# Kernel optimization log

Hardware: AMD Instinct MI355X
Metric: run time of the kernel (lower is better)

Reference implementation:

```python
import jax, jax.numpy as jnp
import numpy as np

N_NODES = 50000
N_EDGES = 800000
IN_DIM = 128
HID_DIM = 64
OUT_DIM = 64
NUM_GRAPHS = 512


def setup_inputs() -> dict:
    key = jax.random.key(0)
    ks = jax.random.split(key, 8)
    x = jax.random.normal(ks[0], (N_NODES, IN_DIM), dtype=jnp.float32)
    edge_index = jax.random.randint(ks[1], (2, N_EDGES), 0, N_NODES, dtype=jnp.int64)
    batch = jnp.sort(jax.random.randint(ks[2], (N_NODES,), 0, NUM_GRAPHS, dtype=jnp.int64))
    s1 = 1.0 / np.sqrt(IN_DIM)
    s2 = 1.0 / np.sqrt(HID_DIM)
    W1 = jax.random.uniform(ks[3], (IN_DIM, HID_DIM), jnp.float32, -s1, s1)
    b1 = jax.random.uniform(ks[4], (HID_DIM,), jnp.float32, -s1, s1)
    W2 = jax.random.uniform(ks[5], (HID_DIM, OUT_DIM), jnp.float32, -s2, s2)
    b2 = jax.random.uniform(ks[6], (OUT_DIM,), jnp.float32, -s2, s2)
    return {"x": x, "edge_index": edge_index, "batch": batch,
            "W1": W1, "b1": b1, "W2": W2, "b2": b2}


def _gcn_layer(h, W, b, src, dst, norm, n_nodes):
    # linear transform first (keeps the per-edge gather at output width)
    h = h @ W + b                      # [N, d_out]
    msg = h[src] * norm[:, None]       # [E, d_out] gathered, normalized messages
    agg = jax.ops.segment_sum(msg, dst, num_segments=n_nodes)  # scatter-add
    return jax.nn.relu(agg)


def reference(x, edge_index, batch, W1, b1, W2, b2):
    src, dst = edge_index[0], edge_index[1]
    # symmetric degree normalization: deg^{-1/2}[src] * deg^{-1/2}[dst]
    deg = jax.ops.segment_sum(jnp.ones((src.shape[0],), x.dtype), dst,
                              num_segments=N_NODES)
    dinv = jax.lax.rsqrt(jnp.maximum(deg, 1.0))
    norm = dinv[src] * dinv[dst]       # [E]

    h = _gcn_layer(x, W1, b1, src, dst, norm, N_NODES)   # dropout = identity (eval)
    h = _gcn_layer(h, W2, b2, src, dst, norm, N_NODES)

    # scatter_mean pooling over batch indices
    sums = jax.ops.segment_sum(h, batch, num_segments=NUM_GRAPHS)
    cnts = jax.ops.segment_sum(jnp.ones((N_NODES,), h.dtype), batch,
                               num_segments=NUM_GRAPHS)
    return sums / jnp.maximum(cnts, 1.0)[:, None]        # [NUM_GRAPHS, OUT_DIM]
```

## Files before the change

kernel.cpp:

```cpp
#include <hip/hip_runtime.h>
#include <hip/hip_fp16.h>

#define N_NODES 50000
#define N_EDGES 800000
#define IN_DIM 128
#define HID_DIM 64
#define OUT_DIM 64
#define NUM_GRAPHS 512
#define CAP 64

typedef unsigned short u16;

__global__ __launch_bounds__(256) void gemm1_fill_kernel(
    const float* __restrict__ X, const float* __restrict__ W,
    const float* __restrict__ bias, __half* __restrict__ Yh, int n_nodes,
    const int* __restrict__ src, const int* __restrict__ dst,
    int* __restrict__ cursor, u16* __restrict__ ssorted, int n_edges) {
    __shared__ float xs[16][IN_DIM];
    const int tid = threadIdx.x;
    const int idx = blockIdx.x >> 1;

    if (blockIdx.x & 1) {
        int e = idx * 256 + tid;
        if (e < n_edges) {
            int d = dst[e];
            int pos = atomicAdd(&cursor[d], 1);
            if (pos < CAP)
                __builtin_nontemporal_store((u16)src[e],
                                            &ssorted[(size_t)d * CAP + pos]);
        }
        return;
    }

    const int base = idx * 16;
    const int nvec = 16 * IN_DIM / 4;
    const float4* X4 = reinterpret_cast<const float4*>(X + (size_t)base * IN_DIM);
    float4* xs4 = reinterpret_cast<float4*>(&xs[0][0]);
    for (int i = tid; i < nvec; i += 256) {
        int row = (i * 4) / IN_DIM;
        xs4[i] = (base + row < n_nodes) ? X4[i] : make_float4(0.f, 0.f, 0.f, 0.f);
    }
    __syncthreads();

    const int j = tid & 63;
    const int q = tid >> 6;
    float b = bias[j];
    float a0 = b, a1 = b, a2 = b, a3 = b;
#pragma unroll 4
    for (int k = 0; k < IN_DIM; ++k) {
        float w = W[k * 64 + j];
        a0 += w * xs[q * 4 + 0][k];
        a1 += w * xs[q * 4 + 1][k];
        a2 += w * xs[q * 4 + 2][k];
        a3 += w * xs[q * 4 + 3][k];
    }
    int n0 = base + q * 4;
    if (n0 + 0 < n_nodes) Yh[(size_t)(n0 + 0) * 64 + j] = __float2half(a0);
    if (n0 + 1 < n_nodes) Yh[(size_t)(n0 + 1) * 64 + j] = __float2half(a1);
    if (n0 + 2 < n_nodes) Yh[(size_t)(n0 + 2) * 64 + j] = __float2half(a2);
    if (n0 + 3 < n_nodes) Yh[(size_t)(n0 + 3) * 64 + j] = __float2half(a3);
}

__global__ __launch_bounds__(256) void scale_bounds_kernel(
    __half* __restrict__ H1h, const int* __restrict__ deg,
    float* __restrict__ dinv, int n_nodes,
    const int* __restrict__ batch, int* __restrict__ gstart, int n_graphs) {
    const int tid = threadIdx.x;
    if (blockIdx.x == gridDim.x - 1) {
        for (int g = tid; g <= n_graphs; g += 256) {
            int lo = 0, hi = n_nodes;
            while (lo < hi) {
                int mid = (lo + hi) >> 1;
                if (batch[mid] < g) lo = mid + 1; else hi = mid;
            }
            gstart[g] = lo;
        }
        return;
    }
    __half2* H2 = reinterpret_cast<__half2*>(H1h);
    const size_t base2 = (size_t)blockIdx.x * 512;
#pragma unroll
    for (int k = 0; k < 2; ++k) {
        size_t el = base2 + (size_t)k * 256 + tid;
        int row = (int)(el >> 5);
        if (row < n_nodes) {
            float dv = rsqrtf(fmaxf((float)deg[row], 1.0f));
            float2 f = __half22float2(H2[el]);
            H2[el] = __floats2half2_rn(f.x * dv, f.y * dv);
            if ((el & 31) == 0) dinv[row] = dv;
        }
    }
}

__device__ __forceinline__ void acc_row(const uint4& v, float2& aa, float2& ab,
                                        float2& ac, float2& ad) {
    const __half2* hp = reinterpret_cast<const __half2*>(&v);
    float2 f;
    f = __half22float2(hp[0]); aa.x += f.x; aa.y += f.y;
    f = __half22float2(hp[1]); ab.x += f.x; ab.y += f.y;
    f = __half22float2(hp[2]); ac.x += f.x; ac.y += f.y;
    f = __half22float2(hp[3]); ad.x += f.x; ad.y += f.y;
}

__global__ __launch_bounds__(256) void agg_gemm_kernel(
    const __half* __restrict__ H, const u16* __restrict__ ssorted,
    const int* __restrict__ deg, const float* __restrict__ dinv,
    const float* __restrict__ W, const float* __restrict__ bias,
    __half* __restrict__ Yh, int n_nodes) {
    __shared__ float xs[32][64];
    const int tid = threadIdx.x;
    const int lane = tid & 63;
    const int w = tid >> 6;
    const int lo = lane & 7;
    const int slot = w * 8 + (lane >> 3);
    const int base = blockIdx.x * 32;
    const uint4* H16 = reinterpret_cast<const uint4*>(H);

    int node = base + slot;
    float2 aa = make_float2(0.f, 0.f), ab = make_float2(0.f, 0.f);
    float2 ac = make_float2(0.f, 0.f), ad = make_float2(0.f, 0.f);
    if (node < n_nodes) {
        int dg = min(deg[node], CAP);
        const u16* sp = ssorted + (size_t)node * CAP;
        int i = 0;
        for (; i + 3 < dg; i += 4) {
            ushort4 s4 = *reinterpret_cast<const ushort4*>(sp + i);
            uint4 v0 = H16[(size_t)s4.x * 8 + lo];
            uint4 v1 = H16[(size_t)s4.y * 8 + lo];
            uint4 v2 = H16[(size_t)s4.z * 8 + lo];
            uint4 v3 = H16[(size_t)s4.w * 8 + lo];
            acc_row(v0, aa, ab, ac, ad);
            acc_row(v1, aa, ab, ac, ad);
            acc_row(v2, aa, ab, ac, ad);
            acc_row(v3, aa, ab, ac, ad);
        }
        for (; i < dg; ++i) {
            uint4 v = H16[(size_t)sp[i] * 8 + lo];
            acc_row(v, aa, ab, ac, ad);
        }
        float dv = dinv[node];
        *reinterpret_cast<float4*>(&xs[slot][8 * lo]) =
            make_float4(fmaxf(aa.x * dv, 0.f), fmaxf(aa.y * dv, 0.f),
                        fmaxf(ab.x * dv, 0.f), fmaxf(ab.y * dv, 0.f));
        *reinterpret_cast<float4*>(&xs[slot][8 * lo + 4]) =
            make_float4(fmaxf(ac.x * dv, 0.f), fmaxf(ac.y * dv, 0.f),
                        fmaxf(ad.x * dv, 0.f), fmaxf(ad.y * dv, 0.f));
    } else {
        *reinterpret_cast<float4*>(&xs[slot][8 * lo]) = make_float4(0.f, 0.f, 0.f, 0.f);
        *reinterpret_cast<float4*>(&xs[slot][8 * lo + 4]) = make_float4(0.f, 0.f, 0.f, 0.f);
    }
    __syncthreads();

    float b = bias[lane];
    float c[8];
#pragma unroll
    for (int r = 0; r < 8; ++r) c[r] = b;
#pragma unroll 4
    for (int k = 0; k < 64; ++k) {
        float wv = W[k * 64 + lane];
#pragma unroll
        for (int r = 0; r < 8; ++r) c[r] += wv * xs[w * 8 + r][k];
    }
    int n0 = base + w * 8;
#pragma unroll
    for (int r = 0; r < 8; ++r)
        if (n0 + r < n_nodes)
            Yh[(size_t)(n0 + r) * 64 + lane] = __float2half(c[r] * dinv[n0 + r]);
}

__global__ __launch_bounds__(256) void agg2_pool_kernel(
    const __half* __restrict__ H, const u16* __restrict__ ssorted,
    const int* __restrict__ deg, const float* __restrict__ dinv,
    const int* __restrict__ gstart, float* __restrict__ out) {
    __shared__ float part[32][64];
    const int g = blockIdx.x >> 1;
    const int sbid = blockIdx.x & 1;
    const int tid = threadIdx.x;
    const int lane = tid & 63;
    const int w = tid >> 6;
    const int lo = lane & 7;
    const int slot = w * 8 + (lane >> 3);
    const uint4* H16 = reinterpret_cast<const uint4*>(H);
    const int beg = gstart[g], end = gstart[g + 1];

    float2 pa = make_float2(0.f, 0.f), pb = make_float2(0.f, 0.f);
    float2 pc = make_float2(0.f, 0.f), pd = make_float2(0.f, 0.f);
    for (int node = beg + sbid * 32 + slot; node < end; node += 64) {
        int dg = min(deg[node], CAP);
        const u16* sp = ssorted + (size_t)node * CAP;
        float2 aa = make_float2(0.f, 0.f), ab = make_float2(0.f, 0.f);
        float2 ac = make_float2(0.f, 0.f), ad = make_float2(0.f, 0.f);
        int i = 0;
        for (; i + 3 < dg; i += 4) {
            ushort4 s4 = *reinterpret_cast<const ushort4*>(sp + i);
            uint4 v0 = H16[(size_t)s4.x * 8 + lo];
            uint4 v1 = H16[(size_t)s4.y * 8 + lo];
            uint4 v2 = H16[(size_t)s4.z * 8 + lo];
            uint4 v3 = H16[(size_t)s4.w * 8 + lo];
            acc_row(v0, aa, ab, ac, ad);
            acc_row(v1, aa, ab, ac, ad);
            acc_row(v2, aa, ab, ac, ad);
            acc_row(v3, aa, ab, ac, ad);
        }
        for (; i < dg; ++i) {
            uint4 v = H16[(size_t)sp[i] * 8 + lo];
            acc_row(v, aa, ab, ac, ad);
        }
        float dv = dinv[node];
        pa.x += fmaxf(aa.x * dv, 0.f); pa.y += fmaxf(aa.y * dv, 0.f);
        pb.x += fmaxf(ab.x * dv, 0.f); pb.y += fmaxf(ab.y * dv, 0.f);
        pc.x += fmaxf(ac.x * dv, 0.f); pc.y += fmaxf(ac.y * dv, 0.f);
        pd.x += fmaxf(ad.x * dv, 0.f); pd.y += fmaxf(ad.y * dv, 0.f);
    }
    *reinterpret_cast<float4*>(&part[slot][8 * lo]) = make_float4(pa.x, pa.y, pb.x, pb.y);
    *reinterpret_cast<float4*>(&part[slot][8 * lo + 4]) = make_float4(pc.x, pc.y, pd.x, pd.y);
    __syncthreads();
    if (tid < 64) {
        float s = 0.f;
#pragma unroll
        for (int r = 0; r < 32; ++r) s += part[r][tid];
        atomicAdd(&out[(size_t)g * 64 + tid], s);
    }
}

__global__ void div_kernel(float* __restrict__ out, const int* __restrict__ gstart,
                           int n) {
    int t = blockIdx.x * blockDim.x + threadIdx.x;
    if (t < n) {
        int g = t >> 6;
        out[t] /= fmaxf((float)(gstart[g + 1] - gstart[g]), 1.0f);
    }
}

extern "C" void kernel_launch(void* const* d_in, const int* in_sizes, int n_in,
                              void* d_out, int out_size, void* d_ws, size_t ws_size,
                              hipStream_t stream) {
    const float* x     = (const float*)d_in[0];
    const int*   ei    = (const int*)d_in[1];
    const int*   batch = (const int*)d_in[2];
    const float* W1    = (const float*)d_in[3];
    const float* b1    = (const float*)d_in[4];
    const float* W2    = (const float*)d_in[5];
    const float* b2    = (const float*)d_in[6];
    float* out = (float*)d_out;

    const int* srcp = ei;
    const int* dstp = ei + N_EDGES;

    __half* H1h     = (__half*)d_ws;
    __half* H2h     = H1h + (size_t)N_NODES * 64;
    float*  dinv    = (float*)(H2h + (size_t)N_NODES * 64);
    int*    cursor  = (int*)(dinv + N_NODES);
    u16*    ssorted = (u16*)(cursor + N_NODES);
    int*    gstart  = (int*)(ssorted + (size_t)N_NODES * CAP);

    hipMemsetAsync(cursor, 0, N_NODES * sizeof(int), stream);
    hipMemsetAsync(out, 0, (size_t)NUM_GRAPHS * OUT_DIM * sizeof(float), stream);

    gemm1_fill_kernel<<<2 * ((N_NODES + 15) / 16), 256, 0, stream>>>(
        x, W1, b1, H1h, N_NODES, srcp, dstp, cursor, ssorted, N_EDGES);

    scale_bounds_kernel<<<(N_NODES + 15) / 16 + 1, 256, 0, stream>>>(
        H1h, cursor, dinv, N_NODES, batch, gstart, NUM_GRAPHS);

    agg_gemm_kernel<<<(N_NODES + 31) / 32, 256, 0, stream>>>(
        H1h, ssorted, cursor, dinv, W2, b2, H2h, N_NODES);

    agg2_pool_kernel<<<2 * NUM_GRAPHS, 256, 0, stream>>>(
        H2h, ssorted, cursor, dinv, gstart, out);
    div_kernel<<<(NUM_GRAPHS * OUT_DIM + 255) / 256, 256, 0, stream>>>(
        out, gstart, NUM_GRAPHS * OUT_DIM);
}
```

Before: 181.7 us.

## Replace per-edge global atomics with two-level bucketed CSR build in shared memory

The per-destination global atomic scatter that built the adjacency lists is replaced with a two-pass bucket sort. Fill blocks first histogram 2048 edges into 256-node buckets and reserve space with one global atomic per bucket. A new fine kernel then builds each bucket's adjacency image in shared memory and writes it out coalesced, computing degree and dinv as well. This removes 800k contended global atomics and scattered 2-byte stores, at the cost of an extra kernel launch and an intermediate packed buffer.

```diff
diff --git a/kernel.cpp b/kernel.cpp
--- a/kernel.cpp
+++ b/kernel.cpp
@@ -8,30 +8,53 @@
 #define OUT_DIM 64
 #define NUM_GRAPHS 512
 #define CAP 64
+#define NB 196
+#define BCAP 5120
+#define FILL_T 2048
+#define NFILL ((N_EDGES + FILL_T - 1) / FILL_T)
 
 typedef unsigned short u16;
+typedef unsigned int u32;
 
 __global__ __launch_bounds__(256) void gemm1_fill_kernel(
     const float* __restrict__ X, const float* __restrict__ W,
     const float* __restrict__ bias, __half* __restrict__ Yh, int n_nodes,
     const int* __restrict__ src, const int* __restrict__ dst,
-    int* __restrict__ cursor, u16* __restrict__ ssorted, int n_edges) {
+    int* __restrict__ gcursor, u32* __restrict__ packed, int n_edges) {
     __shared__ float xs[16][IN_DIM];
-    const int tid = threadIdx.x;
+    __shared__ int hist[256], cnt2[256], goffs[256];
+    const int tid = threadIdx.x;
+
+    if (blockIdx.x & 1) {
+        const int fb = blockIdx.x >> 1;
+        if (fb >= NFILL) return;
+        hist[tid] = 0; cnt2[tid] = 0;
+        __syncthreads();
+        const int base = fb * FILL_T;
+        int d[8], s[8];
+#pragma unroll
+        for (int i = 0; i < 8; ++i) {
+            int e = base + i * 256 + tid;
+            if (e < n_edges) {
+                d[i] = dst[e]; s[i] = src[e];
+                atomicAdd(&hist[d[i] >> 8], 1);
+            } else d[i] = -1;
+        }
+        __syncthreads();
+        if (hist[tid] > 0) goffs[tid] = atomicAdd(&gcursor[tid], hist[tid]);
+        __syncthreads();
+#pragma unroll
+        for (int i = 0; i < 8; ++i) {
+            if (d[i] >= 0) {
+                int b = d[i] >> 8;
+                int p = goffs[b] + atomicAdd(&cnt2[b], 1);
+                packed[(size_t)b * BCAP + p] = ((u32)d[i] << 16) | (u32)s[i];
+            }
+        }
+        return;
+    }
+
     const int idx = blockIdx.x >> 1;
-
-    if (blockIdx.x & 1) {
-        int e = idx * 256 + tid;
-        if (e < n_edges) {
-            int d = dst[e];
-            int pos = atomicAdd(&cursor[d], 1);
-            if (pos < CAP)
-                __builtin_nontemporal_store((u16)src[e],
-                                            &ssorted[(size_t)d * CAP + pos]);
-        }
-        return;
-    }
-
     const int base = idx * 16;
     const int nvec = 16 * IN_DIM / 4;
     const float4* X4 = reinterpret_cast<const float4*>(X + (size_t)base * IN_DIM);
@@ -61,9 +84,37 @@
     if (n0 + 3 < n_nodes) Yh[(size_t)(n0 + 3) * 64 + j] = __float2half(a3);
 }
 
+__global__ __launch_bounds__(256) void fine_kernel(
+    const u32* __restrict__ packed, const int* __restrict__ gcursor,
+    u16* __restrict__ ssorted, int* __restrict__ deg, float* __restrict__ dinv) {
+    __shared__ u16 image[256 * CAP];
+    __shared__ int cur[256];
+    const int b = blockIdx.x;
+    const int tid = threadIdx.x;
+    cur[tid] = 0;
+    __syncthreads();
+    const int cnt = gcursor[b];
+    const u32* pp = packed + (size_t)b * BCAP;
+    for (int i = tid; i < cnt; i += 256) {
+        u32 p = pp[i];
+        int dl = (p >> 16) & 255;
+        int pos = atomicAdd(&cur[dl], 1);
+        if (pos < CAP) image[dl * CAP + pos] = (u16)(p & 0xffff);
+    }
+    __syncthreads();
+    const u32* im32 = reinterpret_cast<const u32*>(image);
+    u32* out32 = reinterpret_cast<u32*>(ssorted) + (size_t)b * (256 * CAP / 2);
+    for (int i = tid; i < 256 * CAP / 2; i += 256) out32[i] = im32[i];
+    int d = b * 256 + tid;
+    if (d < N_NODES) {
+        int c = cur[tid];
+        deg[d] = c;
+        dinv[d] = rsqrtf(fmaxf((float)c, 1.0f));
+    }
+}
+
 __global__ __launch_bounds__(256) void scale_bounds_kernel(
-    __half* __restrict__ H1h, const int* __restrict__ deg,
-    float* __restrict__ dinv, int n_nodes,
+    __half* __restrict__ H1h, const float* __restrict__ dinv, int n_nodes,
     const int* __restrict__ batch, int* __restrict__ gstart, int n_graphs) {
     const int tid = threadIdx.x;
     if (blockIdx.x == gridDim.x - 1) {
@@ -84,10 +135,9 @@
         size_t el = base2 + (size_t)k * 256 + tid;
         int row = (int)(el >> 5);
         if (row < n_nodes) {
-            float dv = rsqrtf(fmaxf((float)deg[row], 1.0f));
+            float dv = dinv[row];
             float2 f = __half22float2(H2[el]);
             H2[el] = __floats2half2_rn(f.x * dv, f.y * dv);
-            if ((el & 31) == 0) dinv[row] = dv;
         }
     }
 }
@@ -250,24 +300,28 @@
     __half* H1h     = (__half*)d_ws;
     __half* H2h     = H1h + (size_t)N_NODES * 64;
     float*  dinv    = (float*)(H2h + (size_t)N_NODES * 64);
-    int*    cursor  = (int*)(dinv + N_NODES);
-    u16*    ssorted = (u16*)(cursor + N_NODES);
-    int*    gstart  = (int*)(ssorted + (size_t)N_NODES * CAP);
-
-    hipMemsetAsync(cursor, 0, N_NODES * sizeof(int), stream);
+    int*    deg     = (int*)(dinv + N_NODES);
+    u16*    ssorted = (u16*)(deg + N_NODES);
+    u32*    packed  = (u32*)(ssorted + (size_t)NB * 256 * CAP);
+    int*    gcursor = (int*)(packed + (size_t)NB * BCAP);
+    int*    gstart  = gcursor + 256;
+
+    hipMemsetAsync(gcursor, 0, 256 * sizeof(int), stream);
     hipMemsetAsync(out, 0, (size_t)NUM_GRAPHS * OUT_DIM * sizeof(float), stream);
 
     gemm1_fill_kernel<<<2 * ((N_NODES + 15) / 16), 256, 0, stream>>>(
-        x, W1, b1, H1h, N_NODES, srcp, dstp, cursor, ssorted, N_EDGES);
+        x, W1, b1, H1h, N_NODES, srcp, dstp, gcursor, packed, N_EDGES);
+
+    fine_kernel<<<NB, 256, 0, stream>>>(packed, gcursor, ssorted, deg, dinv);
 
     scale_bounds_kernel<<<(N_NODES + 15) / 16 + 1, 256, 0, stream>>>(
-        H1h, cursor, dinv, N_NODES, batch, gstart, NUM_GRAPHS);
+        H1h, dinv, N_NODES, batch, gstart, NUM_GRAPHS);
 
     agg_gemm_kernel<<<(N_NODES + 31) / 32, 256, 0, stream>>>(
-        H1h, ssorted, cursor, dinv, W2, b2, H2h, N_NODES);
+        H1h, ssorted, deg, dinv, W2, b2, H2h, N_NODES);
 
     agg2_pool_kernel<<<2 * NUM_GRAPHS, 256, 0, stream>>>(
-        H2h, ssorted, cursor, dinv, gstart, out);
+        H2h, ssorted, deg, dinv, gstart, out);
     div_kernel<<<(NUM_GRAPHS * OUT_DIM + 255) / 256, 256, 0, stream>>>(
         out, gstart, NUM_GRAPHS * OUT_DIM);
 }
```

New measurement: 185.6 us. 1.02x slower.
